# Kernel optimization log

Measured on AMD Instinct MI355X. Metric: run time of the kernel, lower is better.

Reference implementation:

```python
import jax, jax.numpy as jnp
import numpy as np

N_NODES = 50000
N_EDGES = 800000


def sage_conv(x, src, dst, Wl, b, Wr, n_nodes):
    # mean aggregation of source-node features into target nodes
    msg = x[src]                                            # [E, d]
    agg = jax.ops.segment_sum(msg, dst, num_segments=n_nodes)  # [N, d]
    cnt = jax.ops.segment_sum(jnp.ones((src.shape[0],), x.dtype), dst,
                              num_segments=n_nodes)         # [N]
    agg = agg / jnp.maximum(cnt, 1.0)[:, None]
    # out = lin_l(mean_aggr) + lin_r(x); bias only on lin_l (PyG default)
    return agg @ Wl.T + b + x @ Wr.T


def setup_inputs() -> dict:
    key = jax.random.key(0)
    ks = jax.random.split(key, 10)
    d_in, d_h, d_out = 128, 128, 64
    sc = lambda k, shp: jax.random.normal(k, shp, jnp.float32) * (1.0 / np.sqrt(shp[-1]))
    return {
        "x": jax.random.normal(ks[0], (N_NODES, d_in), jnp.float32),
        "edge_index": jax.random.randint(ks[1], (2, N_EDGES), 0, N_NODES, jnp.int64),
        "W1l": sc(ks[2], (d_h, d_in)), "b1": jnp.zeros((d_h,), jnp.float32),
        "W1r": sc(ks[3], (d_h, d_in)),
        "W2l": sc(ks[4], (d_h, d_h)), "b2": jnp.zeros((d_h,), jnp.float32),
        "W2r": sc(ks[5], (d_h, d_h)),
        "W3l": sc(ks[6], (d_out, d_h)), "b3": jnp.zeros((d_out,), jnp.float32),
        "W3r": sc(ks[7], (d_out, d_h)),
    }


def reference(x, edge_index, W1l, b1, W1r, W2l, b2, W2r, W3l, b3, W3r):
    src, dst = edge_index[0], edge_index[1]
    n = x.shape[0]
    # layer 1 + relu (dropout is identity in eval mode)
    h = jax.nn.relu(sage_conv(x, src, dst, W1l, b1, W1r, n))
    # layer 2 + relu
    h = jax.nn.relu(sage_conv(h, src, dst, W2l, b2, W2r, n))
    # final layer, no activation
    return sage_conv(h, src, dst, W3l, b3, W3r, n)
```

## Files before the change

kernel.cpp:

```cpp
#include <hip/hip_runtime.h>
#include <hip/hip_bf16.h>

#define DIN 128

typedef __attribute__((ext_vector_type(8))) short short8;
typedef __attribute__((ext_vector_type(4))) float f32x4;
typedef __attribute__((ext_vector_type(4))) unsigned short ushort4v;
typedef __attribute__((ext_vector_type(8))) unsigned short ushort8v;

__device__ __forceinline__ unsigned short f2bf(float f) {
    unsigned int u = __float_as_uint(f);
    u += 0x7FFFu + ((u >> 16) & 1u);
    return (unsigned short)(u >> 16);
}
__device__ __forceinline__ float bflo(unsigned int v) { return __uint_as_float(v << 16); }
__device__ __forceinline__ float bfhi(unsigned int v) { return __uint_as_float(v & 0xFFFF0000u); }

#define PAD 32
#define CHUNK 4096
#define LCOL 4096
#define BCAP 8192

__device__ __forceinline__ void pack_w_body(const float* __restrict__ Wl,
                                            const float* __restrict__ Wr,
                                            unsigned short* __restrict__ Wp, int NT, int idx) {
    if (idx >= NT * 8 * 64) return;
    int l = idx & 63;
    int ts = idx >> 6;
    int ks = ts & 7;
    int nt = ts >> 3;
    int row = nt * 16 + (l & 15);
    int k = ks * 32 + ((l >> 4) << 3);
    const float* s = (k < 128) ? (Wl + (size_t)row * 128 + k)
                               : (Wr + (size_t)row * 128 + (k - 128));
    float4 v0 = *reinterpret_cast<const float4*>(s);
    float4 v1 = *reinterpret_cast<const float4*>(s + 4);
    unsigned short* d = Wp + (size_t)idx * 8;
    ushort4v o0 = {f2bf(v0.x), f2bf(v0.y), f2bf(v0.z), f2bf(v0.w)};
    ushort4v o1 = {f2bf(v1.x), f2bf(v1.y), f2bf(v1.z), f2bf(v1.w)};
    *reinterpret_cast<ushort4v*>(d) = o0;
    *reinterpret_cast<ushort4v*>(d + 4) = o1;
}

__global__ __launch_bounds__(256) void prep_kernel(
    const float* __restrict__ x, unsigned short* __restrict__ xb,
    const float* __restrict__ W1l, const float* __restrict__ W1r, unsigned short* __restrict__ Wp1,
    const float* __restrict__ W2l, const float* __restrict__ W2r, unsigned short* __restrict__ Wp2,
    const float* __restrict__ W3l, const float* __restrict__ W3r, unsigned short* __restrict__ Wp3,
    int n, int CB) {
    int t = threadIdx.x;
    int b = blockIdx.x;
    if (b < CB) {
        int i = b * 256 + t;
        if (i < n * 16) {
            int node = i >> 4;
            int f0 = (i & 15) << 3;
            const float* s = x + (size_t)node * DIN + f0;
            float4 v0 = *reinterpret_cast<const float4*>(s);
            float4 v1 = *reinterpret_cast<const float4*>(s + 4);
            ushort8v o = {f2bf(v0.x), f2bf(v0.y), f2bf(v0.z), f2bf(v0.w),
                          f2bf(v1.x), f2bf(v1.y), f2bf(v1.z), f2bf(v1.w)};
            *reinterpret_cast<ushort8v*>(xb + (size_t)(f0 >> 5) * n * 32 +
                                         (size_t)node * 32 + (f0 & 31)) = o;
        }
        return;
    }
    b -= CB;
    if (b < 16) { pack_w_body(W1l, W1r, Wp1, 8, b * 256 + t); return; }
    b -= 16;
    if (b < 16) { pack_w_body(W2l, W2r, Wp2, 8, b * 256 + t); return; }
    b -= 16;
    if (b < 8) { pack_w_body(W3l, W3r, Wp3, 4, b * 256 + t); return; }
}

__global__ __launch_bounds__(256) void chunk_scatter_kernel(const int* __restrict__ src,
                                                            const int* __restrict__ dst,
                                                            int* __restrict__ bcur,
                                                            unsigned int* __restrict__ tmp,
                                                            int E) {
    __shared__ int base[256];
    __shared__ int hist[256];
    int t = threadIdx.x;
    int e0 = blockIdx.x * CHUNK;
    int e1 = min(e0 + CHUNK, E);
    hist[t] = 0;
    __syncthreads();
    for (int e = e0 + t; e < e1; e += 256) {
        atomicAdd(&hist[dst[e] >> 8], 1);
    }
    __syncthreads();
    int hh = hist[t];
    if (hh > 0) base[t] = atomicAdd(&bcur[t * PAD], hh);
    __syncthreads();
    hist[t] = 0;
    __syncthreads();
    for (int e = e0 + t; e < e1; e += 256) {
        int d = dst[e];
        int bb = d >> 8;
        int p = base[bb] + atomicAdd(&hist[bb], 1);
        if (p < BCAP)
            tmp[(size_t)bb * BCAP + p] =
                (unsigned int)src[e] | ((unsigned int)(d & 255) << 16);
    }
}

__global__ __launch_bounds__(256) void bucket_fill_kernel(const unsigned int* __restrict__ tmp,
                                                          const int* __restrict__ bcur,
                                                          int* __restrict__ row_ptr,
                                                          unsigned short* __restrict__ col,
                                                          int n, int nb_total, int E) {
    int b = blockIdx.x;
    int node0 = b << 8;
    int nn = min(256, n - node0);
    __shared__ int sc[256];
    __shared__ int cur[256];
    int t = threadIdx.x;
    int v = (t < nb_total) ? min(bcur[t * PAD], BCAP) : 0;
    sc[t] = v;
    __syncthreads();
    for (int off = 1; off < 256; off <<= 1) {
        int add = (t >= off) ? sc[t - off] : 0;
        __syncthreads();
        sc[t] += add;
        __syncthreads();
    }
    int begB = (b == 0) ? 0 : sc[b - 1];
    int sizeB = sc[b] - begB;
    __syncthreads();
    const unsigned int* reg = tmp + (size_t)b * BCAP;
    sc[t] = 0;
    __syncthreads();
    for (int i = t; i < sizeB; i += 256)
        atomicAdd(&sc[(reg[i] >> 16) & 255], 1);
    __syncthreads();
    int dv = sc[t];
    __syncthreads();
    for (int off = 1; off < 256; off <<= 1) {
        int add = (t >= off) ? sc[t - off] : 0;
        __syncthreads();
        sc[t] += add;
        __syncthreads();
    }
    int r = begB + sc[t] - dv;
    if (t < nn) row_ptr[node0 + t] = r;
    cur[t] = r;
    __syncthreads();
    for (int i = t; i < sizeB; i += 256) {
        unsigned int e = reg[i];
        int p = atomicAdd(&cur[(e >> 16) & 255], 1);
        col[p] = (unsigned short)(e & 0xFFFFu);
    }
    if (b == 0 && t == 0) row_ptr[n] = E;
}

__global__ __launch_bounds__(256) void aggregate_kernel(const unsigned short* __restrict__ feat,
                                                        const int* __restrict__ row_ptr,
                                                        const unsigned short* __restrict__ col,
                                                        unsigned short* __restrict__ agg,
                                                        int n) {
    __shared__ unsigned short lcol[LCOL];
    int b = blockIdx.x;
    int chunk = (b >> 1) & 3;
    int nb = (b >> 3) * 2 + (b & 1);
    int node0 = nb * 16;
    if (node0 >= n) return;
    int nend = min(node0 + 16, n);
    int t = threadIdx.x;
    int e0 = row_ptr[node0];
    int ecnt = row_ptr[nend] - e0;
    bool inlds = (ecnt <= LCOL);
    if (inlds) {
        for (int i = t; i < ecnt; i += 256) lcol[i] = col[e0 + i];
    }
    __syncthreads();

    int lane = t & 63;
    int wave = t >> 6;
    int q = lane >> 4;
    int node = node0 + wave * 4 + q;
    int slot = (lane >> 2) & 3;
    int fb = (lane & 3) << 3;
    size_t cs = (size_t)n * 32;
    const unsigned short* fc = feat + (size_t)chunk * cs;

    int beg = 0, end = 0;
    if (node < n) { beg = row_ptr[node]; end = row_ptr[node + 1]; }
    float a0 = 0.f, a1 = 0.f, a2 = 0.f, a3 = 0.f, a4 = 0.f, a5 = 0.f, a6 = 0.f, a7 = 0.f;
    int e = beg + slot;
    if (inlds) {
        for (; e + 12 < end; e += 16) {
            int c0 = lcol[e - e0];
            int c1 = lcol[e + 4 - e0];
            int c2 = lcol[e + 8 - e0];
            int c3 = lcol[e + 12 - e0];
            uint4 v0 = *reinterpret_cast<const uint4*>(fc + (size_t)c0 * 32 + fb);
            uint4 v1 = *reinterpret_cast<const uint4*>(fc + (size_t)c1 * 32 + fb);
            uint4 v2 = *reinterpret_cast<const uint4*>(fc + (size_t)c2 * 32 + fb);
            uint4 v3 = *reinterpret_cast<const uint4*>(fc + (size_t)c3 * 32 + fb);
            a0 += bflo(v0.x); a1 += bfhi(v0.x); a2 += bflo(v0.y); a3 += bfhi(v0.y);
            a4 += bflo(v0.z); a5 += bfhi(v0.z); a6 += bflo(v0.w); a7 += bfhi(v0.w);
            a0 += bflo(v1.x); a1 += bfhi(v1.x); a2 += bflo(v1.y); a3 += bfhi(v1.y);
            a4 += bflo(v1.z); a5 += bfhi(v1.z); a6 += bflo(v1.w); a7 += bfhi(v1.w);
            a0 += bflo(v2.x); a1 += bfhi(v2.x); a2 += bflo(v2.y); a3 += bfhi(v2.y);
            a4 += bflo(v2.z); a5 += bfhi(v2.z); a6 += bflo(v2.w); a7 += bfhi(v2.w);
            a0 += bflo(v3.x); a1 += bfhi(v3.x); a2 += bflo(v3.y); a3 += bfhi(v3.y);
            a4 += bflo(v3.z); a5 += bfhi(v3.z); a6 += bflo(v3.w); a7 += bfhi(v3.w);
        }
        for (; e < end; e += 4) {
            int c0 = lcol[e - e0];
            uint4 v0 = *reinterpret_cast<const uint4*>(fc + (size_t)c0 * 32 + fb);
            a0 += bflo(v0.x); a1 += bfhi(v0.x); a2 += bflo(v0.y); a3 += bfhi(v0.y);
            a4 += bflo(v0.z); a5 += bfhi(v0.z); a6 += bflo(v0.w); a7 += bfhi(v0.w);
        }
    } else {
        for (; e < end; e += 4) {
            int c0 = col[e];
            uint4 v0 = *reinterpret_cast<const uint4*>(fc + (size_t)c0 * 32 + fb);
            a0 += bflo(v0.x); a1 += bfhi(v0.x); a2 += bflo(v0.y); a3 += bfhi(v0.y);
            a4 += bflo(v0.z); a5 += bfhi(v0.z); a6 += bflo(v0.w); a7 += bfhi(v0.w);
        }
    }
    a0 += __shfl_xor(a0, 4); a1 += __shfl_xor(a1, 4); a2 += __shfl_xor(a2, 4);
    a3 += __shfl_xor(a3, 4); a4 += __shfl_xor(a4, 4); a5 += __shfl_xor(a5, 4);
    a6 += __shfl_xor(a6, 4); a7 += __shfl_xor(a7, 4);
    a0 += __shfl_xor(a0, 8); a1 += __shfl_xor(a1, 8); a2 += __shfl_xor(a2, 8);
    a3 += __shfl_xor(a3, 8); a4 += __shfl_xor(a4, 8); a5 += __shfl_xor(a5, 8);
    a6 += __shfl_xor(a6, 8); a7 += __shfl_xor(a7, 8);
    if (slot == 0 && node < n) {
        float sc = 1.0f / fmaxf((float)(end - beg), 1.0f);
        ushort8v o = {f2bf(a0 * sc), f2bf(a1 * sc), f2bf(a2 * sc), f2bf(a3 * sc),
                      f2bf(a4 * sc), f2bf(a5 * sc), f2bf(a6 * sc), f2bf(a7 * sc)};
        *reinterpret_cast<ushort8v*>(agg + (size_t)chunk * cs + (size_t)node * 32 + fb) = o;
    }
}

__global__ __launch_bounds__(256, 4) void mfma_gemm_kernel(
    const unsigned short* __restrict__ aggb, const unsigned short* __restrict__ xb,
    const unsigned short* __restrict__ Wp, const float* __restrict__ bias,
    unsigned short* __restrict__ outv, int n) {
    constexpr int NT = 8;
    const int lane = threadIdx.x & 63;
    const int wave = threadIdx.x >> 6;
    const int row0 = blockIdx.x * 64 + wave * 16;
    const int ar = row0 + (lane & 15);
    const int kg = (lane >> 4) << 3;
    const bool ok = ar < n;
    const size_t cs = (size_t)n * 32;

    const short8 z = {0, 0, 0, 0, 0, 0, 0, 0};
    short8 a[8];
    const unsigned short* arow = aggb + (size_t)ar * 32 + kg;
    const unsigned short* xrow = xb + (size_t)ar * 32 + kg;
#pragma unroll
    for (int ks = 0; ks < 4; ks++)
        a[ks] = ok ? *reinterpret_cast<const short8*>(arow + ks * cs) : z;
#pragma unroll
    for (int ks = 0; ks < 4; ks++)
        a[4 + ks] = ok ? *reinterpret_cast<const short8*>(xrow + ks * cs) : z;

    f32x4 acc[NT];
#pragma unroll
    for (int nt = 0; nt < NT; nt++) acc[nt] = {0.f, 0.f, 0.f, 0.f};

    const unsigned short* wp = Wp + ((size_t)lane << 3);
#pragma unroll
    for (int nt = 0; nt < NT; nt++) {
#pragma unroll
        for (int ks = 0; ks < 8; ks++) {
            short8 b = *reinterpret_cast<const short8*>(wp + ((size_t)(nt * 8 + ks) << 9));
            acc[nt] = __builtin_amdgcn_mfma_f32_16x16x32_bf16(a[ks], b, acc[nt], 0, 0, 0);
        }
    }

    const int orow0 = row0 + ((lane >> 4) << 2);
#pragma unroll
    for (int nt = 0; nt < NT; nt++) {
        int c = nt * 16 + (lane & 15);
        float bv = bias[c];
#pragma unroll
        for (int rg = 0; rg < 4; rg++) {
            int rr = orow0 + rg;
            if (rr < n) {
                float v = fmaxf(acc[nt][rg] + bv, 0.f);
                outv[(size_t)(nt >> 1) * cs + (size_t)rr * 32 + ((nt & 1) * 16 + (lane & 15))] =
                    f2bf(v);
            }
        }
    }
}

__global__ __launch_bounds__(256, 4) void gemm3_kernel(
    const unsigned short* __restrict__ h2, const unsigned short* __restrict__ Wp3,
    const float* __restrict__ bias, unsigned short* __restrict__ y3l,
    float* __restrict__ y3r, int n) {
    const int lane = threadIdx.x & 63;
    const int wave = threadIdx.x >> 6;
    const int row0 = blockIdx.x * 64 + wave * 16;
    const int ar = row0 + (lane & 15);
    const int kg = (lane >> 4) << 3;
    const bool ok = ar < n;
    const size_t cs = (size_t)n * 32;

    const short8 z = {0, 0, 0, 0, 0, 0, 0, 0};
    short8 a[4];
    const unsigned short* xrow = h2 + (size_t)ar * 32 + kg;
#pragma unroll
    for (int ks = 0; ks < 4; ks++)
        a[ks] = ok ? *reinterpret_cast<const short8*>(xrow + ks * cs) : z;

    f32x4 accL[4], accR[4];
#pragma unroll
    for (int nt = 0; nt < 4; nt++) { accL[nt] = {0.f, 0.f, 0.f, 0.f}; accR[nt] = {0.f, 0.f, 0.f, 0.f}; }

    const unsigned short* wp = Wp3 + ((size_t)lane << 3);
#pragma unroll
    for (int nt = 0; nt < 4; nt++) {
#pragma unroll
        for (int ks = 0; ks < 4; ks++) {
            short8 bl = *reinterpret_cast<const short8*>(wp + ((size_t)(nt * 8 + ks) << 9));
            accL[nt] = __builtin_amdgcn_mfma_f32_16x16x32_bf16(a[ks], bl, accL[nt], 0, 0, 0);
            short8 br = *reinterpret_cast<const short8*>(wp + ((size_t)(nt * 8 + 4 + ks) << 9));
            accR[nt] = __builtin_amdgcn_mfma_f32_16x16x32_bf16(a[ks], br, accR[nt], 0, 0, 0);
        }
    }

    const int orow0 = row0 + ((lane >> 4) << 2);
#pragma unroll
    for (int nt = 0; nt < 4; nt++) {
        int c = nt * 16 + (lane & 15);
        float bv = bias[c];
#pragma unroll
        for (int rg = 0; rg < 4; rg++) {
            int rr = orow0 + rg;
            if (rr < n) {
                y3l[(size_t)(nt >> 1) * cs + (size_t)rr * 32 + ((nt & 1) * 16 + (lane & 15))] =
                    f2bf(accL[nt][rg]);
                y3r[(size_t)rr * 64 + c] = accR[nt][rg] + bv;
            }
        }
    }
}

__global__ __launch_bounds__(256) void agg_add_kernel(const unsigned short* __restrict__ y3l,
                                                      const float* __restrict__ y3r,
                                                      const int* __restrict__ row_ptr,
                                                      const unsigned short* __restrict__ col,
                                                      float* __restrict__ out, int n) {
    __shared__ unsigned short lcol[LCOL];
    int b = blockIdx.x;
    int chunk = (b >> 2) & 1;
    int nb = (b >> 3) * 4 + (b & 3);
    int node0 = nb * 16;
    if (node0 >= n) return;
    int nend = min(node0 + 16, n);
    int t = threadIdx.x;
    int e0 = row_ptr[node0];
    int ecnt = row_ptr[nend] - e0;
    bool inlds = (ecnt <= LCOL);
    if (inlds) {
        for (int i = t; i < ecnt; i += 256) lcol[i] = col[e0 + i];
    }
    __syncthreads();

    int lane = t & 63;
    int wave = t >> 6;
    int q = lane >> 4;
    int node = node0 + wave * 4 + q;
    int slot = (lane >> 2) & 3;
    int fb = (lane & 3) << 3;
    size_t cs = (size_t)n * 32;
    const unsigned short* fc = y3l + (size_t)chunk * cs;

    int beg = 0, end = 0;
    if (node < n) { beg = row_ptr[node]; end = row_ptr[node + 1]; }
    float a0 = 0.f, a1 = 0.f, a2 = 0.f, a3 = 0.f, a4 = 0.f, a5 = 0.f, a6 = 0.f, a7 = 0.f;
    int e = beg + slot;
    if (inlds) {
        for (; e + 12 < end; e += 16) {
            int c0 = lcol[e - e0];
            int c1 = lcol[e + 4 - e0];
            int c2 = lcol[e + 8 - e0];
            int c3 = lcol[e + 12 - e0];
            uint4 v0 = *reinterpret_cast<const uint4*>(fc + (size_t)c0 * 32 + fb);
            uint4 v1 = *reinterpret_cast<const uint4*>(fc + (size_t)c1 * 32 + fb);
            uint4 v2 = *reinterpret_cast<const uint4*>(fc + (size_t)c2 * 32 + fb);
            uint4 v3 = *reinterpret_cast<const uint4*>(fc + (size_t)c3 * 32 + fb);
            a0 += bflo(v0.x); a1 += bfhi(v0.x); a2 += bflo(v0.y); a3 += bfhi(v0.y);
            a4 += bflo(v0.z); a5 += bfhi(v0.z); a6 += bflo(v0.w); a7 += bfhi(v0.w);
            a0 += bflo(v1.x); a1 += bfhi(v1.x); a2 += bflo(v1.y); a3 += bfhi(v1.y);
            a4 += bflo(v1.z); a5 += bfhi(v1.z); a6 += bflo(v1.w); a7 += bfhi(v1.w);
            a0 += bflo(v2.x); a1 += bfhi(v2.x); a2 += bflo(v2.y); a3 += bfhi(v2.y);
            a4 += bflo(v2.z); a5 += bfhi(v2.z); a6 += bflo(v2.w); a7 += bfhi(v2.w);
            a0 += bflo(v3.x); a1 += bfhi(v3.x); a2 += bflo(v3.y); a3 += bfhi(v3.y);
            a4 += bflo(v3.z); a5 += bfhi(v3.z); a6 += bflo(v3.w); a7 += bfhi(v3.w);
        }
        for (; e < end; e += 4) {
            int c0 = lcol[e - e0];
            uint4 v0 = *reinterpret_cast<const uint4*>(fc + (size_t)c0 * 32 + fb);
            a0 += bflo(v0.x); a1 += bfhi(v0.x); a2 += bflo(v0.y); a3 += bfhi(v0.y);
            a4 += bflo(v0.z); a5 += bfhi(v0.z); a6 += bflo(v0.w); a7 += bfhi(v0.w);
        }
    } else {
        for (; e < end; e += 4) {
            int c0 = col[e];
            uint4 v0 = *reinterpret_cast<const uint4*>(fc + (size_t)c0 * 32 + fb);
            a0 += bflo(v0.x); a1 += bfhi(v0.x); a2 += bflo(v0.y); a3 += bfhi(v0.y);
            a4 += bflo(v0.z); a5 += bfhi(v0.z); a6 += bflo(v0.w); a7 += bfhi(v0.w);
        }
    }
    a0 += __shfl_xor(a0, 4); a1 += __shfl_xor(a1, 4); a2 += __shfl_xor(a2, 4);
    a3 += __shfl_xor(a3, 4); a4 += __shfl_xor(a4, 4); a5 += __shfl_xor(a5, 4);
    a6 += __shfl_xor(a6, 4); a7 += __shfl_xor(a7, 4);
    a0 += __shfl_xor(a0, 8); a1 += __shfl_xor(a1, 8); a2 += __shfl_xor(a2, 8);
    a3 += __shfl_xor(a3, 8); a4 += __shfl_xor(a4, 8); a5 += __shfl_xor(a5, 8);
    a6 += __shfl_xor(a6, 8); a7 += __shfl_xor(a7, 8);
    if (slot == 0 && node < n) {
        float sc = 1.0f / fmaxf((float)(end - beg), 1.0f);
        const float* yr = y3r + (size_t)node * 64 + chunk * 32 + fb;
        float* o = out + (size_t)node * 64 + chunk * 32 + fb;
        float4 r0 = make_float4(a0 * sc + yr[0], a1 * sc + yr[1], a2 * sc + yr[2], a3 * sc + yr[3]);
        float4 r1 = make_float4(a4 * sc + yr[4], a5 * sc + yr[5], a6 * sc + yr[6], a7 * sc + yr[7]);
        *reinterpret_cast<float4*>(o) = r0;
        *reinterpret_cast<float4*>(o + 4) = r1;
    }
}

extern "C" void kernel_launch(void* const* d_in, const int* in_sizes, int n_in,
                              void* d_out, int out_size, void* d_ws, size_t ws_size,
                              hipStream_t stream) {
    const float* x = (const float*)d_in[0];
    const int* ei = (const int*)d_in[1];
    const float* W1l = (const float*)d_in[2];
    const float* b1 = (const float*)d_in[3];
    const float* W1r = (const float*)d_in[4];
    const float* W2l = (const float*)d_in[5];
    const float* b2 = (const float*)d_in[6];
    const float* W2r = (const float*)d_in[7];
    const float* W3l = (const float*)d_in[8];
    const float* b3 = (const float*)d_in[9];
    const float* W3r = (const float*)d_in[10];
    float* out = (float*)d_out;

    const int n = in_sizes[0] / DIN;
    const int E = in_sizes[1] / 2;
    const int* src = ei;
    const int* dst = ei + E;

    char* p = (char*)d_ws;
    auto take = [&](size_t bytes) {
        char* r = p;
        p += (bytes + 255) & ~(size_t)255;
        return r;
    };
    int* bcur = (int*)take(256 * PAD * 4);
    int* row_ptr = (int*)take(((size_t)n + 1) * 4);
    unsigned int* tmp = (unsigned int*)take((size_t)256 * BCAP * 4);
    unsigned short* col = (unsigned short*)take((size_t)E * 2 + 512);
    unsigned short* xb = (unsigned short*)take((size_t)n * DIN * 2);
    unsigned short* aggb = (unsigned short*)take((size_t)n * DIN * 2);
    unsigned short* h1b = (unsigned short*)take((size_t)n * DIN * 2);
    unsigned short* h2b = (unsigned short*)take((size_t)n * DIN * 2);
    unsigned short* y3l = (unsigned short*)take((size_t)n * 64 * 2);
    float* y3r = (float*)take((size_t)n * 64 * 4);
    unsigned short* Wp1 = (unsigned short*)take(128 * 256 * 2);
    unsigned short* Wp2 = (unsigned short*)take(128 * 256 * 2);
    unsigned short* Wp3 = (unsigned short*)take(64 * 256 * 2);

    const int n_buckets = (n + 255) / 256;
    const int nbn = (n + 15) / 16;
    const int nbn2 = (nbn + 1) & ~1;
    const int nb_agg = 4 * nbn2;
    const int nbn4 = (nbn + 3) & ~3;
    const int nb_agg3 = 2 * nbn4;
    const int nb_gemm = (n + 63) / 64;
    const int nb_chunk = (E + CHUNK - 1) / CHUNK;
    const int CB = (n * 16 + 255) / 256;
    const int nb_prep = CB + 16 + 16 + 8;

    hipMemsetAsync(bcur, 0, 256 * PAD * 4, stream);
    prep_kernel<<<nb_prep, 256, 0, stream>>>(x, xb, W1l, W1r, Wp1, W2l, W2r, Wp2,
                                             W3l, W3r, Wp3, n, CB);

    chunk_scatter_kernel<<<nb_chunk, 256, 0, stream>>>(src, dst, bcur, tmp, E);
    bucket_fill_kernel<<<n_buckets, 256, 0, stream>>>(tmp, bcur, row_ptr, col, n, n_buckets, E);

    aggregate_kernel<<<nb_agg, 256, 0, stream>>>(xb, row_ptr, col, aggb, n);
    mfma_gemm_kernel<<<nb_gemm, 256, 0, stream>>>(aggb, xb, Wp1, b1, h1b, n);

    aggregate_kernel<<<nb_agg, 256, 0, stream>>>(h1b, row_ptr, col, aggb, n);
    mfma_gemm_kernel<<<nb_gemm, 256, 0, stream>>>(aggb, h1b, Wp2, b2, h2b, n);

    gemm3_kernel<<<nb_gemm, 256, 0, stream>>>(h2b, Wp3, b3, y3l, y3r, n);
    agg_add_kernel<<<nb_agg3, 256, 0, stream>>>(y3l, y3r, row_ptr, col, out, n);
}
```

Measured before the change: 167.6 us.

## Merge prep and edge-scatter kernels; double rows per wave in MFMA GEMMs

After: 190.5 us. +13.7%, slower.

```diff
diff --git a/kernel.cpp b/kernel.cpp
--- a/kernel.cpp
+++ b/kernel.cpp
@@ -42,12 +42,16 @@
     *reinterpret_cast<ushort4v*>(d + 4) = o1;
 }
 
-__global__ __launch_bounds__(256) void prep_kernel(
+__global__ __launch_bounds__(256) void prep_scatter_kernel(
     const float* __restrict__ x, unsigned short* __restrict__ xb,
     const float* __restrict__ W1l, const float* __restrict__ W1r, unsigned short* __restrict__ Wp1,
     const float* __restrict__ W2l, const float* __restrict__ W2r, unsigned short* __restrict__ Wp2,
     const float* __restrict__ W3l, const float* __restrict__ W3r, unsigned short* __restrict__ Wp3,
-    int n, int CB) {
+    const int* __restrict__ src, const int* __restrict__ dst,
+    int* __restrict__ bcur, unsigned int* __restrict__ tmp,
+    int E, int n, int CB) {
+    __shared__ int base[256];
+    __shared__ int hist[256];
     int t = threadIdx.x;
     int b = blockIdx.x;
     if (b < CB) {
@@ -71,18 +75,10 @@
     if (b < 16) { pack_w_body(W2l, W2r, Wp2, 8, b * 256 + t); return; }
     b -= 16;
     if (b < 8) { pack_w_body(W3l, W3r, Wp3, 4, b * 256 + t); return; }
-}
-
-__global__ __launch_bounds__(256) void chunk_scatter_kernel(const int* __restrict__ src,
-                                                            const int* __restrict__ dst,
-                                                            int* __restrict__ bcur,
-                                                            unsigned int* __restrict__ tmp,
-                                                            int E) {
-    __shared__ int base[256];
-    __shared__ int hist[256];
-    int t = threadIdx.x;
-    int e0 = blockIdx.x * CHUNK;
+    b -= 8;
+    int e0 = b * CHUNK;
     int e1 = min(e0 + CHUNK, E);
+    if (e0 >= E) return;
     hist[t] = 0;
     __syncthreads();
     for (int e = e0 + t; e < e1; e += 256) {
@@ -234,33 +230,46 @@
     }
 }
 
-__global__ __launch_bounds__(256, 4) void mfma_gemm_kernel(
+__global__ __launch_bounds__(256, 2) void mfma_gemm_kernel(
     const unsigned short* __restrict__ aggb, const unsigned short* __restrict__ xb,
     const unsigned short* __restrict__ Wp, const float* __restrict__ bias,
     unsigned short* __restrict__ outv, int n) {
     constexpr int NT = 8;
     const int lane = threadIdx.x & 63;
     const int wave = threadIdx.x >> 6;
-    const int row0 = blockIdx.x * 64 + wave * 16;
-    const int ar = row0 + (lane & 15);
+    const int row0 = blockIdx.x * 128 + wave * 32;
+    const int ar0 = row0 + (lane & 15);
+    const int ar1 = ar0 + 16;
     const int kg = (lane >> 4) << 3;
-    const bool ok = ar < n;
+    const bool ok0 = ar0 < n;
+    const bool ok1 = ar1 < n;
     const size_t cs = (size_t)n * 32;
 
     const short8 z = {0, 0, 0, 0, 0, 0, 0, 0};
-    short8 a[8];
-    const unsigned short* arow = aggb + (size_t)ar * 32 + kg;
-    const unsigned short* xrow = xb + (size_t)ar * 32 + kg;
-#pragma unroll
-    for (int ks = 0; ks < 4; ks++)
-        a[ks] = ok ? *reinterpret_cast<const short8*>(arow + ks * cs) : z;
-#pragma unroll
-    for (int ks = 0; ks < 4; ks++)
-        a[4 + ks] = ok ? *reinterpret_cast<const short8*>(xrow + ks * cs) : z;
-
-    f32x4 acc[NT];
-#pragma unroll
-    for (int nt = 0; nt < NT; nt++) acc[nt] = {0.f, 0.f, 0.f, 0.f};
+    short8 a0[8], a1[8];
+    {
+        const unsigned short* ag0 = aggb + (size_t)ar0 * 32 + kg;
+        const unsigned short* xr0 = xb + (size_t)ar0 * 32 + kg;
+        const unsigned short* ag1 = aggb + (size_t)ar1 * 32 + kg;
+        const unsigned short* xr1 = xb + (size_t)ar1 * 32 + kg;
+#pragma unroll
+        for (int ks = 0; ks < 4; ks++) {
+            a0[ks] = ok0 ? *reinterpret_cast<const short8*>(ag0 + ks * cs) : z;
+            a1[ks] = ok1 ? *reinterpret_cast<const short8*>(ag1 + ks * cs) : z;
+        }
+#pragma unroll
+        for (int ks = 0; ks < 4; ks++) {
+            a0[4 + ks] = ok0 ? *reinterpret_cast<const short8*>(xr0 + ks * cs) : z;
+            a1[4 + ks] = ok1 ? *reinterpret_cast<const short8*>(xr1 + ks * cs) : z;
+        }
+    }
+
+    f32x4 acc0[NT], acc1[NT];
+#pragma unroll
+    for (int nt = 0; nt < NT; nt++) {
+        acc0[nt] = {0.f, 0.f, 0.f, 0.f};
+        acc1[nt] = {0.f, 0.f, 0.f, 0.f};
+    }
 
     const unsigned short* wp = Wp + ((size_t)lane << 3);
 #pragma unroll
@@ -268,7 +277,8 @@
 #pragma unroll
         for (int ks = 0; ks < 8; ks++) {
             short8 b = *reinterpret_cast<const short8*>(wp + ((size_t)(nt * 8 + ks) << 9));
-            acc[nt] = __builtin_amdgcn_mfma_f32_16x16x32_bf16(a[ks], b, acc[nt], 0, 0, 0);
+            acc0[nt] = __builtin_amdgcn_mfma_f32_16x16x32_bf16(a0[ks], b, acc0[nt], 0, 0, 0);
+            acc1[nt] = __builtin_amdgcn_mfma_f32_16x16x32_bf16(a1[ks], b, acc1[nt], 0, 0, 0);
         }
     }
 
@@ -277,40 +287,57 @@
     for (int nt = 0; nt < NT; nt++) {
         int c = nt * 16 + (lane & 15);
         float bv = bias[c];
+        size_t obase = (size_t)(nt >> 1) * cs + ((nt & 1) * 16 + (lane & 15));
 #pragma unroll
         for (int rg = 0; rg < 4; rg++) {
             int rr = orow0 + rg;
             if (rr < n) {
-                float v = fmaxf(acc[nt][rg] + bv, 0.f);
-                outv[(size_t)(nt >> 1) * cs + (size_t)rr * 32 + ((nt & 1) * 16 + (lane & 15))] =
-                    f2bf(v);
+                float v = fmaxf(acc0[nt][rg] + bv, 0.f);
+                outv[obase + (size_t)rr * 32] = f2bf(v);
             }
-        }
-    }
-}
-
-__global__ __launch_bounds__(256, 4) void gemm3_kernel(
+            int rr1 = rr + 16;
+            if (rr1 < n) {
+                float v = fmaxf(acc1[nt][rg] + bv, 0.f);
+                outv[obase + (size_t)rr1 * 32] = f2bf(v);
+            }
+        }
+    }
+}
+
+__global__ __launch_bounds__(256, 2) void gemm3_kernel(
     const unsigned short* __restrict__ h2, const unsigned short* __restrict__ Wp3,
     const float* __restrict__ bias, unsigned short* __restrict__ y3l,
     float* __restrict__ y3r, int n) {
     const int lane = threadIdx.x & 63;
     const int wave = threadIdx.x >> 6;
-    const int row0 = blockIdx.x * 64 + wave * 16;
-    const int ar = row0 + (lane & 15);
+    const int row0 = blockIdx.x * 128 + wave * 32;
+    const int ar0 = row0 + (lane & 15);
+    const int ar1 = ar0 + 16;
     const int kg = (lane >> 4) << 3;
-    const bool ok = ar < n;
+    const bool ok0 = ar0 < n;
+    const bool ok1 = ar1 < n;
     const size_t cs = (size_t)n * 32;
 
     const short8 z = {0, 0, 0, 0, 0, 0, 0, 0};
-    short8 a[4];
-    const unsigned short* xrow = h2 + (size_t)ar * 32 + kg;
-#pragma unroll
-    for (int ks = 0; ks < 4; ks++)
-        a[ks] = ok ? *reinterpret_cast<const short8*>(xrow + ks * cs) : z;
-
-    f32x4 accL[4], accR[4];
-#pragma unroll
-    for (int nt = 0; nt < 4; nt++) { accL[nt] = {0.f, 0.f, 0.f, 0.f}; accR[nt] = {0.f, 0.f, 0.f, 0.f}; }
+    short8 a0[4], a1[4];
+    {
+        const unsigned short* x0 = h2 + (size_t)ar0 * 32 + kg;
+        const unsigned short* x1 = h2 + (size_t)ar1 * 32 + kg;
+#pragma unroll
+        for (int ks = 0; ks < 4; ks++) {
+            a0[ks] = ok0 ? *reinterpret_cast<const short8*>(x0 + ks * cs) : z;
+            a1[ks] = ok1 ? *reinterpret_cast<const short8*>(x1 + ks * cs) : z;
+        }
+    }
+
+    f32x4 accL0[4], accR0[4], accL1[4], accR1[4];
+#pragma unroll
+    for (int nt = 0; nt < 4; nt++) {
+        accL0[nt] = {0.f, 0.f, 0.f, 0.f};
+        accR0[nt] = {0.f, 0.f, 0.f, 0.f};
+        accL1[nt] = {0.f, 0.f, 0.f, 0.f};
+        accR1[nt] = {0.f, 0.f, 0.f, 0.f};
+    }
 
     const unsigned short* wp = Wp3 + ((size_t)lane << 3);
 #pragma unroll
@@ -318,9 +345,11 @@
 #pragma unroll
         for (int ks = 0; ks < 4; ks++) {
             short8 bl = *reinterpret_cast<const short8*>(wp + ((size_t)(nt * 8 + ks) << 9));
-            accL[nt] = __builtin_amdgcn_mfma_f32_16x16x32_bf16(a[ks], bl, accL[nt], 0, 0, 0);
+            accL0[nt] = __builtin_amdgcn_mfma_f32_16x16x32_bf16(a0[ks], bl, accL0[nt], 0, 0, 0);
+            accL1[nt] = __builtin_amdgcn_mfma_f32_16x16x32_bf16(a1[ks], bl, accL1[nt], 0, 0, 0);
             short8 br = *reinterpret_cast<const short8*>(wp + ((size_t)(nt * 8 + 4 + ks) << 9));
-            accR[nt] = __builtin_amdgcn_mfma_f32_16x16x32_bf16(a[ks], br, accR[nt], 0, 0, 0);
+            accR0[nt] = __builtin_amdgcn_mfma_f32_16x16x32_bf16(a0[ks], br, accR0[nt], 0, 0, 0);
+            accR1[nt] = __builtin_amdgcn_mfma_f32_16x16x32_bf16(a1[ks], br, accR1[nt], 0, 0, 0);
         }
     }
 
@@ -329,13 +358,18 @@
     for (int nt = 0; nt < 4; nt++) {
         int c = nt * 16 + (lane & 15);
         float bv = bias[c];
+        size_t lbase = (size_t)(nt >> 1) * cs + ((nt & 1) * 16 + (lane & 15));
 #pragma unroll
         for (int rg = 0; rg < 4; rg++) {
             int rr = orow0 + rg;
             if (rr < n) {
-                y3l[(size_t)(nt >> 1) * cs + (size_t)rr * 32 + ((nt & 1) * 16 + (lane & 15))] =
-                    f2bf(accL[nt][rg]);
-                y3r[(size_t)rr * 64 + c] = accR[nt][rg] + bv;
+                y3l[lbase + (size_t)rr * 32] = f2bf(accL0[nt][rg]);
+                y3r[(size_t)rr * 64 + c] = accR0[nt][rg] + bv;
+            }
+            int rr1 = rr + 16;
+            if (rr1 < n) {
+                y3l[lbase + (size_t)rr1 * 32] = f2bf(accL1[nt][rg]);
+                y3r[(size_t)rr1 * 64 + c] = accR1[nt][rg] + bv;
             }
         }
     }
@@ -472,16 +506,15 @@
     const int nb_agg = 4 * nbn2;
     const int nbn4 = (nbn + 3) & ~3;
     const int nb_agg3 = 2 * nbn4;
-    const int nb_gemm = (n + 63) / 64;
+    const int nb_gemm = (n + 127) / 128;
     const int nb_chunk = (E + CHUNK - 1) / CHUNK;
     const int CB = (n * 16 + 255) / 256;
-    const int nb_prep = CB + 16 + 16 + 8;
+    const int nb_ps = CB + 16 + 16 + 8 + nb_chunk;
 
     hipMemsetAsync(bcur, 0, 256 * PAD * 4, stream);
-    prep_kernel<<<nb_prep, 256, 0, stream>>>(x, xb, W1l, W1r, Wp1, W2l, W2r, Wp2,
-                                             W3l, W3r, Wp3, n, CB);
-
-    chunk_scatter_kernel<<<nb_chunk, 256, 0, stream>>>(src, dst, bcur, tmp, E);
+    prep_scatter_kernel<<<nb_ps, 256, 0, stream>>>(x, xb, W1l, W1r, Wp1, W2l, W2r, Wp2,
+                                                   W3l, W3r, Wp3, src, dst, bcur, tmp,
+                                                   E, n, CB);
     bucket_fill_kernel<<<n_buckets, 256, 0, stream>>>(tmp, bcur, row_ptr, col, n, n_buckets, E);
 
     aggregate_kernel<<<nb_agg, 256, 0, stream>>>(xb, row_ptr, col, aggb, n);
```
